# Kernel tuning notes

Measured on AMD Instinct MI355X. Metric: run time of the kernel, lower is better.

Reference implementation:

```python
import jax, jax.numpy as jnp
import numpy as np

B, T, P, D, L = 16, 120, 96, 128, 2


def setup_inputs() -> dict:
    key = jax.random.key(0)
    k1, k2, k3, k4 = jax.random.split(key, 4)
    x = jax.random.normal(k1, (B, P, D, T), dtype=jnp.float32)
    # distances: symmetric-ish positive pairwise distances from random 3D points
    pts = jax.random.uniform(k2, (B, T, P, 3), dtype=jnp.float32) * 5.0
    diff = pts[:, :, :, None, :] - pts[:, :, None, :, :]
    distances = jnp.sqrt(jnp.sum(diff * diff, axis=-1) + 1e-12)
    # contiguous-prefix padding mask (matches the original self-loop loop semantics)
    counts = jax.random.randint(k3, (B,), P // 2, P + 1)
    padding_mask = jnp.arange(P)[None, :] < counts[:, None]
    # params: xavier_uniform with gain 1e-5 ~ tiny; bias 0; LN gamma=1, beta=0
    limit = 1e-5 * np.sqrt(6.0 / (D + D))
    W = jax.random.uniform(k4, (L, D, D), minval=-limit, maxval=limit, dtype=jnp.float32)
    b = jnp.zeros((L, D), dtype=jnp.float32)
    gamma = jnp.ones((L, D), dtype=jnp.float32)
    beta = jnp.zeros((L, D), dtype=jnp.float32)
    return {"x": x, "distances": distances, "padding_mask": padding_mask,
            "W": W, "b": b, "gamma": gamma, "beta": beta}


def _build_adjacency(distances, padding_mask):
    # valid_mask: [B,T,P,P]
    vm2d = (padding_mask[:, :, None] & padding_mask[:, None, :]).astype(distances.dtype)  # [B,P,P]
    vm = vm2d[:, None, :, :]
    vd = distances * vm
    pos = (vd > 0).astype(distances.dtype)
    n = jnp.sum(pos)
    mean = jnp.sum(vd * pos) / n
    var = jnp.sum(((vd - mean) ** 2) * pos) / (n - 1.0)  # unbiased, as torch.std
    sigma = jnp.sqrt(var) + 1e-8
    adj = jnp.exp(-(distances ** 2) / (2.0 * sigma ** 2)) * vm
    # self loops on valid (contiguous-prefix) nodes: add diag(mask)
    eye_mask = jnp.eye(P, dtype=distances.dtype)[None, :, :] * padding_mask[:, :, None].astype(distances.dtype)
    adj = adj + eye_mask[:, None, :, :]
    # symmetric normalization D^{-1/2} A D^{-1/2}
    deg = jnp.clip(jnp.sum(adj, axis=-1, keepdims=True), 1e-8, None)  # [B,T,P,1]
    deg = jnp.clip(deg * padding_mask[:, None, :, None].astype(distances.dtype), 1e-8, None)
    dis = deg ** -0.5
    adj = dis * adj * jnp.swapaxes(dis, -2, -1)
    return adj * vm


def _layer_norm_D(x, g, bt, eps=1e-5):
    # x: [B,P,D,T]; normalize over D axis
    mu = jnp.mean(x, axis=2, keepdims=True)
    var = jnp.mean((x - mu) ** 2, axis=2, keepdims=True)
    return (x - mu) * jax.lax.rsqrt(var + eps) * g[None, None, :, None] + bt[None, None, :, None]


def reference(x, distances, padding_mask, W, b, gamma, beta):
    adj = _build_adjacency(distances, padding_mask)  # [B,T,P,P]
    mask_f = padding_mask.astype(x.dtype)
    for l in range(L):
        xt = jnp.transpose(x, (0, 3, 1, 2))                      # [B,T,P,D]
        h = jnp.einsum('btpd,de->btpe', xt, W[l])                # x @ W
        o = jnp.einsum('btpq,btqd->btpd', adj, h)                # A @ xW
        o = jax.nn.relu(o + b[l])
        o = o * mask_f[:, None, :, None]
        o = jnp.transpose(o, (0, 2, 3, 1))                       # [B,P,D,T]
        o = _layer_norm_D(o, gamma[l], beta[l])
        x = x + o
    return x
```

## Files before the change

kernel.cpp:

```cpp
#include <hip/hip_runtime.h>
#include <math.h>

typedef __bf16 bf16_t;
typedef __bf16 bf16x8 __attribute__((ext_vector_type(8)));
typedef __bf16 bf16x4 __attribute__((ext_vector_type(4)));
typedef float f32x4 __attribute__((ext_vector_type(4)));

namespace {
constexpr int kB = 16;
constexpr int kT = 120;
constexpr int kP = 96;
constexpr int kD = 128;
constexpr int kBT = kB * kT;
constexpr int kPP = kP * kP;
constexpr int kPD = kP * kD;
constexpr long long kND = (long long)kBT * kPP;

constexpr int PD_CHUNK = 256;
constexpr int TIN_BLOCKS = kB * 48;
constexpr int PREP_BLOCKS = 128;
constexpr int STATS_BLOCKS = 1024;
constexpr int FRONT_BLOCKS = TIN_BLOCKS + PREP_BLOCKS + STATS_BLOCKS;
constexpr int LROW = PD_CHUNK + 8;
constexpr int TIN_SMEM = kT * LROW * 2;

constexpr int YS = 136;
constexpr int HS = 104;
constexpr int OS = 132;
constexpr int AS = 104;
constexpr int HT_OFF = 26112;
constexpr int AL_OFF = 52736;
constexpr int MROW_OFF = 72704;
constexpr int DIS_OFF = 73088;
constexpr int SMEM_B = 73472;
}

__device__ __forceinline__ f32x4 mfma16(bf16x8 a, bf16x8 b, f32x4 c) {
    return __builtin_amdgcn_mfma_f32_16x16x32_bf16(a, b, c, 0, 0, 0);
}

__global__ __launch_bounds__(256) void k_front(const float* __restrict__ x,
                                               bf16_t* __restrict__ y,
                                               const float* __restrict__ dist,
                                               const unsigned char* __restrict__ mraw,
                                               int* __restrict__ mask,
                                               double* __restrict__ stats,
                                               const float* __restrict__ W,
                                               bf16_t* __restrict__ wT) {
    __shared__ __align__(16) char sm[TIN_SMEM];
    const int bid = blockIdx.x;
    const int tid = threadIdx.x;

    if (bid < TIN_BLOCKS) {
        bf16_t* lds = (bf16_t*)sm;
        int b = bid / 48;
        int pc = bid - b * 48;
        int pd0 = pc * PD_CHUNK;

        {
            const float* rp = x + ((long long)b * kPD + pd0 + tid) * kT;
            #pragma unroll
            for (int c4 = 0; c4 < 30; ++c4) {
                float4 v = *(const float4*)(rp + c4 * 4);
                lds[(c4 * 4 + 0) * LROW + tid] = (bf16_t)v.x;
                lds[(c4 * 4 + 1) * LROW + tid] = (bf16_t)v.y;
                lds[(c4 * 4 + 2) * LROW + tid] = (bf16_t)v.z;
                lds[(c4 * 4 + 3) * LROW + tid] = (bf16_t)v.w;
            }
        }
        __syncthreads();
        bf16_t* yb = y + (long long)b * kT * kPD + pd0;
        #pragma unroll
        for (int k = 0; k < 15; ++k) {
            int idx = k * 256 + tid;
            int t = idx >> 5, c = idx & 31;
            bf16x8 v = *(const bf16x8*)(lds + t * LROW + c * 8);
            *(bf16x8*)(yb + (long long)t * kPD + c * 8) = v;
        }
    } else if (bid < TIN_BLOCKS + PREP_BLOCKS) {
        int pb = bid - TIN_BLOCKS;
        int l = pb >> 6;
        int idx = (pb & 63) * 256 + tid;
        int n = idx >> 7, k = idx & 127;
        wT[l * 16384 + n * 128 + k] = (bf16_t)W[l * 16384 + k * 128 + n];

        if (pb == 0) {
            const unsigned int* u32 = (const unsigned int*)mraw;
            unsigned int w0 = u32[0];
            int mode;
            if (w0 == 0x01010101u) mode = 0;
            else if (w0 == 1u) mode = 1;
            else mode = 2;
            for (int i = tid; i < kB * kP; i += 256) {
                int v;
                if (mode == 0)      v = (mraw[i] != 0);
                else if (mode == 1) v = (u32[i] != 0);
                else                v = (((const float*)mraw)[i] != 0.0f);
                mask[i] = v;
            }
        }
    } else {
        int sb = bid - TIN_BLOCKS - PREP_BLOCKS;
        int* ml = (int*)sm;
        double* sh = (double*)(sm + 6144);
        {
            const unsigned int* u32 = (const unsigned int*)mraw;
            unsigned int w0 = u32[0];
            int mode;
            if (w0 == 0x01010101u) mode = 0;
            else if (w0 == 1u) mode = 1;
            else mode = 2;
            for (int i = tid; i < kB * kP; i += 256) {
                int v;
                if (mode == 0)      v = (mraw[i] != 0);
                else if (mode == 1) v = (u32[i] != 0);
                else                v = (((const float*)mraw)[i] != 0.0f);
                ml[i] = v;
            }
        }
        __syncthreads();

        long long n4 = kND / 4;
        long long stride = (long long)STATS_BLOCKS * 256;
        double s = 0.0, s2 = 0.0;
        int cnt = 0;
        for (long long i4 = (long long)sb * 256 + tid; i4 < n4; i4 += stride) {
            int q0 = 4 * (int)(i4 % 24);
            long long r = i4 / 24;
            int p = (int)(r % 96);
            int b = (int)((r / 96) / kT);
            const int* mb = ml + b * kP;
            if (mb[p]) {
                float4 d4 = *(const float4*)(dist + i4 * 4);
                if (mb[q0 + 0]) { s += d4.x; s2 += (double)d4.x * d4.x; cnt++; }
                if (mb[q0 + 1]) { s += d4.y; s2 += (double)d4.y * d4.y; cnt++; }
                if (mb[q0 + 2]) { s += d4.z; s2 += (double)d4.z * d4.z; cnt++; }
                if (mb[q0 + 3]) { s += d4.w; s2 += (double)d4.w * d4.w; cnt++; }
            }
        }
        sh[tid] = s; __syncthreads();
        for (int off = 128; off > 0; off >>= 1) { if (tid < off) sh[tid] += sh[tid + off]; __syncthreads(); }
        if (tid == 0) atomicAdd(&stats[0], sh[0]);
        __syncthreads();
        sh[tid] = s2; __syncthreads();
        for (int off = 128; off > 0; off >>= 1) { if (tid < off) sh[tid] += sh[tid + off]; __syncthreads(); }
        if (tid == 0) atomicAdd(&stats[1], sh[0]);
        __syncthreads();
        sh[tid] = (double)cnt; __syncthreads();
        for (int off = 128; off > 0; off >>= 1) { if (tid < off) sh[tid] += sh[tid + off]; __syncthreads(); }
        if (tid == 0) atomicAdd(&stats[2], sh[0]);
    }
}

__global__ __launch_bounds__(256) void k_tout(const bf16_t* __restrict__ y,
                                              float* __restrict__ out) {
    __shared__ float tile[64 * 121];
    int b = blockIdx.y, pd0 = blockIdx.x * 64;
    int tid = threadIdx.x;
    const bf16_t* yb = y + (long long)b * kT * kPD + pd0;
    #pragma unroll
    for (int k = 0; k < 4; ++k) {
        int idx = k * 256 + tid;
        if (idx < 960) {
            int t = idx >> 3, dg = idx & 7;
            bf16x8 v = *(const bf16x8*)(yb + (long long)t * kPD + dg * 8);
            #pragma unroll
            for (int j = 0; j < 8; ++j) tile[(dg * 8 + j) * 121 + t] = (float)v[j];
        }
    }
    __syncthreads();
    float* ob = out + ((long long)b * kPD + pd0) * kT;
    #pragma unroll
    for (int k = 0; k < 8; ++k) {
        int idx = k * 256 + tid;
        if (idx < 1920) {
            int r = idx / 30, c = idx - r * 30;
            float4 v;
            v.x = tile[r * 121 + c * 4 + 0];
            v.y = tile[r * 121 + c * 4 + 1];
            v.z = tile[r * 121 + c * 4 + 2];
            v.w = tile[r * 121 + c * 4 + 3];
            *(float4*)(ob + r * kT + c * 4) = v;
        }
    }
}

__global__ __launch_bounds__(512, 2) void k_gcn(bf16_t* __restrict__ y,
                                                const float* __restrict__ dist,
                                                const int* __restrict__ mask,
                                                const double* __restrict__ stats,
                                                const bf16_t* __restrict__ wT,
                                                const float* __restrict__ bias,
                                                const float* __restrict__ gamma,
                                                const float* __restrict__ beta) {
    __shared__ __align__(16) char smem[SMEM_B];
    bf16_t* yL  = (bf16_t*)smem;
    bf16_t* hT  = (bf16_t*)(smem + HT_OFF);
    bf16_t* oLb = (bf16_t*)(smem + HT_OFF);
    float*  aT  = (float*)smem;
    bf16_t* aL  = (bf16_t*)(smem + AL_OFF);
    float* mrowf = (float*)(smem + MROW_OFF);
    float* dis   = (float*)(smem + DIS_OFF);

    const int tid = threadIdx.x;
    const int tx = tid & 15, ty = tid >> 4;
    const int lane = tid & 63, w = tid >> 6;
    const int wm = w >> 2, wn = w & 3;
    const int fc = lane & 15, fg = lane >> 4;
    const int bt = blockIdx.x, b = bt / kT;
    const int d0 = tx * 8;

    bf16_t* ybt = y + (size_t)bt * kPD;
    const float* dbt = dist + (size_t)bt * kPP;

    if (tid < kP) mrowf[tid] = (float)mask[b * kP + tid];

    double sn = stats[2];
    double mean = stats[0] / sn;
    double var = (stats[1] - sn * mean * mean) / (sn - 1.0);
    double sg = sqrt(var) + 1e-8;
    float inv2s2 = (float)(1.0 / (2.0 * sg * sg));

    __syncthreads();

    #pragma unroll
    for (int k = 0; k < 5; ++k) {
        int i4 = k * 512 + tid;
        if (i4 < 2304) {
            int e = i4 * 4;
            int p = e / kP, q = e - p * kP;
            float4 d4 = *(const float4*)(dbt + e);
            float mp = mrowf[p];
            float vv[4];
            vv[0] = (mp * mrowf[q + 0] != 0.f) ? __expf(-d4.x * d4.x * inv2s2) : 0.f;
            vv[1] = (mp * mrowf[q + 1] != 0.f) ? __expf(-d4.y * d4.y * inv2s2) : 0.f;
            vv[2] = (mp * mrowf[q + 2] != 0.f) ? __expf(-d4.z * d4.z * inv2s2) : 0.f;
            vv[3] = (mp * mrowf[q + 3] != 0.f) ? __expf(-d4.w * d4.w * inv2s2) : 0.f;
            #pragma unroll
            for (int j = 0; j < 4; ++j) {
                if (p == q + j) vv[j] += mp;
                aT[p * 100 + q + j] = vv[j];
            }
        }
    }
    __syncthreads();

    if (tid < kP) {
        float s = 0.f;
        for (int q = 0; q < kP; ++q) s += aT[q * 100 + tid];
        s = fmaxf(s, 1e-8f);
        s = fmaxf(s * mrowf[tid], 1e-8f);
        dis[tid] = rsqrtf(s);
    }
    __syncthreads();

    #pragma unroll
    for (int k = 0; k < 5; ++k) {
        int i4 = k * 512 + tid;
        if (i4 < 2304) {
            int e = i4 * 4;
            int p = e / kP, q = e - p * kP;
            float dp = dis[p];
            bf16x4 ov;
            #pragma unroll
            for (int j = 0; j < 4; ++j)
                ov[j] = (bf16_t)(dp * aT[p * 100 + q + j] * dis[q + j]);
            *(bf16x4*)(aL + p * AS + q) = ov;
        }
    }
    __syncthreads();

    #pragma unroll
    for (int i = 0; i < 3; ++i) {
        int p = ty * 3 + i;
        *(bf16x8*)(yL + p * YS + d0) = *(const bf16x8*)(ybt + p * kD + d0);
    }

    for (int l = 0; l < 2; ++l) {
        const bf16_t* wTl = wT + l * kD * kD;
        bf16x8 wf[4][2];
        #pragma unroll
        for (int kt = 0; kt < 4; ++kt) {
            wf[kt][0] = *(const bf16x8*)(wTl + ((wn * 2 + 0) * 16 + fc) * kD + kt * 32 + fg * 8);
            wf[kt][1] = *(const bf16x8*)(wTl + ((wn * 2 + 1) * 16 + fc) * kD + kt * 32 + fg * 8);
        }
        __syncthreads();

        f32x4 acc[3][2];
        #pragma unroll
        for (int mt = 0; mt < 3; ++mt) { acc[mt][0] = {0,0,0,0}; acc[mt][1] = {0,0,0,0}; }
        #pragma unroll
        for (int kt = 0; kt < 4; ++kt) {
            #pragma unroll
            for (int mt = 0; mt < 3; ++mt) {
                bf16x8 af = *(const bf16x8*)(yL + ((wm * 3 + mt) * 16 + fc) * YS + kt * 32 + fg * 8);
                acc[mt][0] = mfma16(af, wf[kt][0], acc[mt][0]);
                acc[mt][1] = mfma16(af, wf[kt][1], acc[mt][1]);
            }
        }
        #pragma unroll
        for (int mt = 0; mt < 3; ++mt)
            #pragma unroll
            for (int nn = 0; nn < 2; ++nn) {
                int e = (wn * 2 + nn) * 16 + fc;
                int p0 = (wm * 3 + mt) * 16 + fg * 4;
                bf16x4 hv = {(bf16_t)acc[mt][nn][0], (bf16_t)acc[mt][nn][1],
                             (bf16_t)acc[mt][nn][2], (bf16_t)acc[mt][nn][3]};
                *(bf16x4*)(hT + e * HS + p0) = hv;
            }
        __syncthreads();

        f32x4 acc2[3][2];
        #pragma unroll
        for (int mt = 0; mt < 3; ++mt) { acc2[mt][0] = {0,0,0,0}; acc2[mt][1] = {0,0,0,0}; }
        #pragma unroll
        for (int kt = 0; kt < 3; ++kt) {
            bf16x8 bf0 = *(const bf16x8*)(hT + ((wn * 2 + 0) * 16 + fc) * HS + kt * 32 + fg * 8);
            bf16x8 bf1 = *(const bf16x8*)(hT + ((wn * 2 + 1) * 16 + fc) * HS + kt * 32 + fg * 8);
            #pragma unroll
            for (int mt = 0; mt < 3; ++mt) {
                bf16x8 af = *(const bf16x8*)(aL + ((wm * 3 + mt) * 16 + fc) * AS + kt * 32 + fg * 8);
                acc2[mt][0] = mfma16(af, bf0, acc2[mt][0]);
                acc2[mt][1] = mfma16(af, bf1, acc2[mt][1]);
            }
        }
        __syncthreads();

        #pragma unroll
        for (int mt = 0; mt < 3; ++mt)
            #pragma unroll
            for (int nn = 0; nn < 2; ++nn) {
                int d = (wn * 2 + nn) * 16 + fc;
                int p0 = (wm * 3 + mt) * 16 + fg * 4;
                oLb[(p0 + 0) * OS + d] = (bf16_t)acc2[mt][nn][0];
                oLb[(p0 + 1) * OS + d] = (bf16_t)acc2[mt][nn][1];
                oLb[(p0 + 2) * OS + d] = (bf16_t)acc2[mt][nn][2];
                oLb[(p0 + 3) * OS + d] = (bf16_t)acc2[mt][nn][3];
            }
        __syncthreads();

        const float* bl = bias + l * kD;
        const float* gl = gamma + l * kD;
        const float* bel = beta + l * kD;
        float4 bb0 = *(const float4*)(bl + d0), bb1 = *(const float4*)(bl + d0 + 4);
        float4 gg0 = *(const float4*)(gl + d0), gg1 = *(const float4*)(gl + d0 + 4);
        float4 be0 = *(const float4*)(bel + d0), be1 = *(const float4*)(bel + d0 + 4);
        float bb[8] = {bb0.x, bb0.y, bb0.z, bb0.w, bb1.x, bb1.y, bb1.z, bb1.w};
        float gg[8] = {gg0.x, gg0.y, gg0.z, gg0.w, gg1.x, gg1.y, gg1.z, gg1.w};
        float be[8] = {be0.x, be0.y, be0.z, be0.w, be1.x, be1.y, be1.z, be1.w};

        #pragma unroll
        for (int i = 0; i < 3; ++i) {
            int p = ty * 3 + i;
            float mpf = mrowf[p];
            bf16x4 o0 = *(const bf16x4*)(oLb + p * OS + d0);
            bf16x4 o1 = *(const bf16x4*)(oLb + p * OS + d0 + 4);
            bf16x8 yv = *(const bf16x8*)(yL + p * YS + d0);
            float v[8];
            #pragma unroll
            for (int j = 0; j < 4; ++j) {
                v[j]     = fmaxf((float)o0[j] + bb[j], 0.f) * mpf;
                v[j + 4] = fmaxf((float)o1[j] + bb[j + 4], 0.f) * mpf;
            }
            float s = v[0] + v[1] + v[2] + v[3] + v[4] + v[5] + v[6] + v[7];
            s += __shfl_xor(s, 8);
            s += __shfl_xor(s, 4);
            s += __shfl_xor(s, 2);
            s += __shfl_xor(s, 1);
            float mu = s * 0.0078125f;

            float ss = 0.f;
            #pragma unroll
            for (int j = 0; j < 8; ++j) { float dv = v[j] - mu; ss += dv * dv; }
            ss += __shfl_xor(ss, 8);
            ss += __shfl_xor(ss, 4);
            ss += __shfl_xor(ss, 2);
            ss += __shfl_xor(ss, 1);
            float inv = rsqrtf(ss * 0.0078125f + 1e-5f);

            bf16x8 c;
            #pragma unroll
            for (int j = 0; j < 8; ++j)
                c[j] = (bf16_t)((float)yv[j] + (v[j] - mu) * inv * gg[j] + be[j]);

            if (l == 0) {
                *(bf16x8*)(yL + p * YS + d0) = c;
            } else {
                *(bf16x8*)(ybt + p * kD + d0) = c;
            }
        }
    }
}

extern "C" void kernel_launch(void* const* d_in, const int* in_sizes, int n_in,
                              void* d_out, int out_size, void* d_ws, size_t ws_size,
                              hipStream_t stream) {
    (void)in_sizes; (void)n_in; (void)out_size; (void)ws_size;

    const float* x = (const float*)d_in[0];
    const float* dist = (const float*)d_in[1];
    const unsigned char* mraw = (const unsigned char*)d_in[2];
    const float* W = (const float*)d_in[3];
    const float* bias = (const float*)d_in[4];
    const float* gamma = (const float*)d_in[5];
    const float* beta = (const float*)d_in[6];
    float* out = (float*)d_out;

    char* ws = (char*)d_ws;
    double* stats = (double*)ws;
    int* mask = (int*)(ws + 64);
    bf16_t* wT = (bf16_t*)(ws + 8192);
    bf16_t* y = (bf16_t*)(ws + 81920);

    hipMemsetAsync(stats, 0, 32, stream);

    k_front<<<FRONT_BLOCKS, 256, 0, stream>>>(x, y, dist, mraw, mask, stats, W, wT);

    k_gcn<<<kBT, 512, 0, stream>>>(y, dist, mask, stats, wT, bias, gamma, beta);

    k_tout<<<dim3(kPD / 64, kB), 256, 0, stream>>>(y, out);
}
```

Baseline: 183.5 us.

## Fuse input transpose into GCN kernel via strided gathers and remap block order

Removes the separate transpose-to-bf16 stage in the front kernel. Each GCN block now gathers its x slice straight from global memory with a T-strided access and converts it to bf16 in LDS, so the bf16 intermediate is no longer written and re-read. The block index is remapped so that neighbouring blocks handle consecutive t values, which lets their strided loads share cache lines. Some __syncthreads are replaced with an explicit lgkmcnt wait plus s_barrier. The risk is that uncoalesced 4-byte gathers hit at 480-byte stride and depend on L2/MALL reuse across concurrently running blocks.

New measurement: 234.7 us. 1.28x slower.

```diff
diff --git a/kernel.cpp b/kernel.cpp
--- a/kernel.cpp
+++ b/kernel.cpp
@@ -16,13 +16,9 @@
 constexpr int kPD = kP * kD;
 constexpr long long kND = (long long)kBT * kPP;
 
-constexpr int PD_CHUNK = 256;
-constexpr int TIN_BLOCKS = kB * 48;
 constexpr int PREP_BLOCKS = 128;
 constexpr int STATS_BLOCKS = 1024;
-constexpr int FRONT_BLOCKS = TIN_BLOCKS + PREP_BLOCKS + STATS_BLOCKS;
-constexpr int LROW = PD_CHUNK + 8;
-constexpr int TIN_SMEM = kT * LROW * 2;
+constexpr int FRONT_BLOCKS = PREP_BLOCKS + STATS_BLOCKS;
 
 constexpr int YS = 136;
 constexpr int HS = 104;
@@ -39,46 +35,24 @@
     return __builtin_amdgcn_mfma_f32_16x16x32_bf16(a, b, c, 0, 0, 0);
 }
 
-__global__ __launch_bounds__(256) void k_front(const float* __restrict__ x,
-                                               bf16_t* __restrict__ y,
-                                               const float* __restrict__ dist,
+__device__ __forceinline__ void bar_lgkm() {
+    asm volatile("s_waitcnt lgkmcnt(0)" ::: "memory");
+    __builtin_amdgcn_s_barrier();
+    __builtin_amdgcn_sched_barrier(0);
+}
+
+__global__ __launch_bounds__(256) void k_front(const float* __restrict__ dist,
                                                const unsigned char* __restrict__ mraw,
                                                int* __restrict__ mask,
                                                double* __restrict__ stats,
                                                const float* __restrict__ W,
                                                bf16_t* __restrict__ wT) {
-    __shared__ __align__(16) char sm[TIN_SMEM];
+    __shared__ __align__(16) char sm[8192];
     const int bid = blockIdx.x;
     const int tid = threadIdx.x;
 
-    if (bid < TIN_BLOCKS) {
-        bf16_t* lds = (bf16_t*)sm;
-        int b = bid / 48;
-        int pc = bid - b * 48;
-        int pd0 = pc * PD_CHUNK;
-
-        {
-            const float* rp = x + ((long long)b * kPD + pd0 + tid) * kT;
-            #pragma unroll
-            for (int c4 = 0; c4 < 30; ++c4) {
-                float4 v = *(const float4*)(rp + c4 * 4);
-                lds[(c4 * 4 + 0) * LROW + tid] = (bf16_t)v.x;
-                lds[(c4 * 4 + 1) * LROW + tid] = (bf16_t)v.y;
-                lds[(c4 * 4 + 2) * LROW + tid] = (bf16_t)v.z;
-                lds[(c4 * 4 + 3) * LROW + tid] = (bf16_t)v.w;
-            }
-        }
-        __syncthreads();
-        bf16_t* yb = y + (long long)b * kT * kPD + pd0;
-        #pragma unroll
-        for (int k = 0; k < 15; ++k) {
-            int idx = k * 256 + tid;
-            int t = idx >> 5, c = idx & 31;
-            bf16x8 v = *(const bf16x8*)(lds + t * LROW + c * 8);
-            *(bf16x8*)(yb + (long long)t * kPD + c * 8) = v;
-        }
-    } else if (bid < TIN_BLOCKS + PREP_BLOCKS) {
-        int pb = bid - TIN_BLOCKS;
+    if (bid < PREP_BLOCKS) {
+        int pb = bid;
         int l = pb >> 6;
         int idx = (pb & 63) * 256 + tid;
         int n = idx >> 7, k = idx & 127;
@@ -100,7 +74,7 @@
             }
         }
     } else {
-        int sb = bid - TIN_BLOCKS - PREP_BLOCKS;
+        int sb = bid - PREP_BLOCKS;
         int* ml = (int*)sm;
         double* sh = (double*)(sm + 6144);
         {
@@ -185,7 +159,8 @@
     }
 }
 
-__global__ __launch_bounds__(512, 2) void k_gcn(bf16_t* __restrict__ y,
+__global__ __launch_bounds__(512, 2) void k_gcn(const float* __restrict__ x,
+                                                bf16_t* __restrict__ y,
                                                 const float* __restrict__ dist,
                                                 const int* __restrict__ mask,
                                                 const double* __restrict__ stats,
@@ -207,11 +182,23 @@
     const int lane = tid & 63, w = tid >> 6;
     const int wm = w >> 2, wn = w & 3;
     const int fc = lane & 15, fg = lane >> 4;
-    const int bt = blockIdx.x, b = bt / kT;
+    const int blk = blockIdx.x;
+    const int bt = (blk & 7) * 240 + (blk >> 3);
+    const int b = bt / kT, t = bt - (bt / kT) * kT;
     const int d0 = tx * 8;
 
     bf16_t* ybt = y + (size_t)bt * kPD;
     const float* dbt = dist + (size_t)bt * kPP;
+
+    float xg[3][8];
+    {
+        const float* xb = x + (((long long)b * kP + ty * 3) * kD + d0) * kT + t;
+        #pragma unroll
+        for (int i = 0; i < 3; ++i)
+            #pragma unroll
+            for (int j = 0; j < 8; ++j)
+                xg[i][j] = xb[(i * kD + j) * kT];
+    }
 
     if (tid < kP) mrowf[tid] = (float)mask[b * kP + tid];
 
@@ -221,7 +208,7 @@
     double sg = sqrt(var) + 1e-8;
     float inv2s2 = (float)(1.0 / (2.0 * sg * sg));
 
-    __syncthreads();
+    bar_lgkm();
 
     #pragma unroll
     for (int k = 0; k < 5; ++k) {
@@ -243,7 +230,7 @@
             }
         }
     }
-    __syncthreads();
+    bar_lgkm();
 
     if (tid < kP) {
         float s = 0.f;
@@ -252,7 +239,7 @@
         s = fmaxf(s * mrowf[tid], 1e-8f);
         dis[tid] = rsqrtf(s);
     }
-    __syncthreads();
+    bar_lgkm();
 
     #pragma unroll
     for (int k = 0; k < 5; ++k) {
@@ -268,12 +255,14 @@
             *(bf16x4*)(aL + p * AS + q) = ov;
         }
     }
-    __syncthreads();
+    bar_lgkm();
 
     #pragma unroll
     for (int i = 0; i < 3; ++i) {
-        int p = ty * 3 + i;
-        *(bf16x8*)(yL + p * YS + d0) = *(const bf16x8*)(ybt + p * kD + d0);
+        bf16x8 c;
+        #pragma unroll
+        for (int j = 0; j < 8; ++j) c[j] = (bf16_t)xg[i][j];
+        *(bf16x8*)(yL + (ty * 3 + i) * YS + d0) = c;
     }
 
     for (int l = 0; l < 2; ++l) {
@@ -414,9 +403,9 @@
 
     hipMemsetAsync(stats, 0, 32, stream);
 
-    k_front<<<FRONT_BLOCKS, 256, 0, stream>>>(x, y, dist, mraw, mask, stats, W, wT);
-
-    k_gcn<<<kBT, 512, 0, stream>>>(y, dist, mask, stats, wT, bias, gamma, beta);
+    k_front<<<FRONT_BLOCKS, 256, 0, stream>>>(dist, mraw, mask, stats, W, wT);
+
+    k_gcn<<<kBT, 512, 0, stream>>>(x, y, dist, mask, stats, wT, bias, gamma, beta);
 
     k_tout<<<dim3(kPD / 64, kB), 256, 0, stream>>>(y, out);
 }
```
